# Kernel optimization log

Measured on AMD Instinct MI355X. Metric: run time of the kernel, lower is better.

Reference implementation:

```python
import jax, jax.numpy as jnp
import numpy as np

B = 1048576      # batch
D = 6            # action dim (x[0]..x[5] in the cvxpy program)
SDIM = 17        # state dim (s[11]..s[16] used)
CAP = 20.0       # constraint radius
BIG = 1e30


def setup_inputs() -> dict:
    key = jax.random.key(0)
    k1, k2 = jax.random.split(key)
    x = jax.random.normal(k1, (B, D), dtype=jnp.float32)
    s = jax.random.normal(k2, (B, SDIM), dtype=jnp.float32)
    return {"x": x, "s": s}


def _project_weighted_l1(q, s):
    # QP: argmin_x 0.5||x||^2 - q^T x  s.t.  sum_i |s[11+i]| * |x_i| <= CAP
    # == Euclidean projection of q onto weighted-L1 ball {x : sum_i w_i|x_i| <= CAP}
    # Closed form: x_i = sign(q_i) * max(|q_i| - lam * w_i, 0), lam >= 0 chosen so
    # constraint is tight (lam = 0 if q is already feasible).
    w = jnp.abs(s[:, 11:11 + D])                       # [B,D] weights
    a = jnp.abs(q)                                     # [B,D]
    sgn = jnp.sign(q)
    total = jnp.sum(w * a, axis=-1, keepdims=True)     # [B,1] constraint value at x=q

    # breakpoints r_i = |q_i| / w_i (coord i active iff r_i > lam); w_i==0 => always q_i
    w_safe = jnp.where(w > 0, w, 1.0)
    r = jnp.where(w > 0, a / w_safe, jnp.float32(BIG))  # [B,D]

    order = jnp.argsort(-r, axis=-1)                   # descending breakpoints
    r_s = jnp.take_along_axis(r, order, axis=-1)
    w_s = jnp.take_along_axis(w, order, axis=-1)
    a_s = jnp.take_along_axis(a, order, axis=-1)

    cum_wq = jnp.cumsum(w_s * a_s, axis=-1)            # [B,D]
    cum_w2 = jnp.cumsum(w_s * w_s, axis=-1)            # [B,D]
    cum_w2_safe = jnp.where(cum_w2 > 0, cum_w2, 1.0)
    lam_k = (cum_wq - CAP) / cum_w2_safe               # candidate lam for prefix k+1

    valid = (r_s > lam_k) & (cum_w2 > 0)               # prefix-monotone validity
    k_star = jnp.maximum(jnp.sum(valid.astype(jnp.int32), axis=-1, keepdims=True) - 1, 0)
    lam = jnp.take_along_axis(lam_k, k_star, axis=-1)  # [B,1]
    lam = jnp.where(total > CAP, jnp.maximum(lam, 0.0), 0.0)

    return sgn * jnp.maximum(a - lam * w, 0.0)         # [B,D]


def reference(x, s):
    return _project_weighted_l1(x, s)
```

## Files before the change

kernel.cpp:

```cpp
#include <hip/hip_runtime.h>

#define DD 6
#define SDIM 17
#define CAPF 20.0f
#define BIGF 1e30f
#define ROWS 256

__global__ __launch_bounds__(256) void proj_wl1_kernel(
    const float* __restrict__ x, const float* __restrict__ s,
    float* __restrict__ out, int B)
{
    __shared__ float ls[ROWS * SDIM];
    __shared__ float lx[ROWS * DD];

    const int tid = threadIdx.x;
    const size_t row0 = (size_t)blockIdx.x * ROWS;
    const bool full = (row0 + ROWS) <= (size_t)B;

    float q[DD], w[DD];

    if (full) {
        const float4* gs = reinterpret_cast<const float4*>(s + row0 * SDIM);
        float4* lsv = reinterpret_cast<float4*>(ls);
        for (int t = tid; t < ROWS * SDIM / 4; t += ROWS) lsv[t] = gs[t];

        const float4* gx = reinterpret_cast<const float4*>(x + row0 * DD);
        float4* lxv = reinterpret_cast<float4*>(lx);
        for (int t = tid; t < ROWS * DD / 4; t += ROWS) lxv[t] = gx[t];

        __syncthreads();

#pragma unroll
        for (int i = 0; i < DD; ++i) q[i] = lx[tid * DD + i];
#pragma unroll
        for (int i = 0; i < DD; ++i) w[i] = fabsf(ls[tid * SDIM + 11 + i]);
    } else {
        size_t row = row0 + tid;
        bool ok = row < (size_t)B;
        const float* xp = x + row * DD;
        const float* sp = s + row * SDIM + 11;
#pragma unroll
        for (int i = 0; i < DD; ++i) q[i] = ok ? xp[i] : 0.f;
#pragma unroll
        for (int i = 0; i < DD; ++i) w[i] = ok ? fabsf(sp[i]) : 0.f;
    }

    float a[DD], r[DD], wq[DD], w2[DD];
    float total = 0.f;
#pragma unroll
    for (int i = 0; i < DD; ++i) {
        a[i]  = fabsf(q[i]);
        wq[i] = w[i] * a[i];
        w2[i] = w[i] * w[i];
        total += wq[i];
        r[i]  = (w[i] > 0.f) ? (a[i] / w[i]) : BIGF;
    }

#pragma unroll
    for (int i = 0; i < DD - 1; ++i) {
#pragma unroll
        for (int j = 0; j < DD - 1 - i; ++j) {
            bool sw = r[j] < r[j + 1];
            float t0 = r[j], t1 = wq[j], t2 = w2[j];
            r[j]  = sw ? r[j + 1]  : r[j];
            wq[j] = sw ? wq[j + 1] : wq[j];
            w2[j] = sw ? w2[j + 1] : w2[j];
            r[j + 1]  = sw ? t0 : r[j + 1];
            wq[j + 1] = sw ? t1 : wq[j + 1];
            w2[j + 1] = sw ? t2 : w2[j + 1];
        }
    }

    float cwq = 0.f, cw2 = 0.f;
    float lamk[DD];
    int m = 0;
#pragma unroll
    for (int k = 0; k < DD; ++k) {
        cwq += wq[k];
        cw2 += w2[k];
        float safe = (cw2 > 0.f) ? cw2 : 1.f;
        lamk[k] = (cwq - CAPF) / safe;
        bool valid = (r[k] > lamk[k]) && (cw2 > 0.f);
        m += valid ? 1 : 0;
    }
    int ks = m - 1;
    if (ks < 0) ks = 0;
    float lam = lamk[0];
#pragma unroll
    for (int k = 1; k < DD; ++k) lam = (ks == k) ? lamk[k] : lam;
    lam = (total > CAPF) ? fmaxf(lam, 0.f) : 0.f;

    float o[DD];
#pragma unroll
    for (int i = 0; i < DD; ++i) {
        float mag = fmaxf(a[i] - lam * w[i], 0.f);
        float sgn = (q[i] > 0.f) ? 1.f : ((q[i] < 0.f) ? -1.f : 0.f);
        o[i] = sgn * mag;
    }

    if (full) {
        __syncthreads();
#pragma unroll
        for (int i = 0; i < DD; ++i) lx[tid * DD + i] = o[i];
        __syncthreads();

        float4* gout = reinterpret_cast<float4*>(out + row0 * DD);
        const float4* lxv = reinterpret_cast<const float4*>(lx);
        for (int t = tid; t < ROWS * DD / 4; t += ROWS) gout[t] = lxv[t];
    } else {
        size_t row = row0 + tid;
        if (row < (size_t)B) {
            float* op = out + row * DD;
#pragma unroll
            for (int i = 0; i < DD; ++i) op[i] = o[i];
        }
    }
}

extern "C" void kernel_launch(void* const* d_in, const int* in_sizes, int n_in,
                              void* d_out, int out_size, void* d_ws, size_t ws_size,
                              hipStream_t stream)
{
    const float* x = (const float*)d_in[0];
    const float* s = (const float*)d_in[1];
    float* out = (float*)d_out;
    int B = in_sizes[0] / DD;

    const int block = ROWS;
    int grid = (B + block - 1) / block;
    proj_wl1_kernel<<<grid, block, 0, stream>>>(x, s, out, B);
}
```

Baseline: 26.78 us.

## Use per-wavefront LDS slabs and drop block barriers; load x directly as float2

Each 64-lane wavefront now stages its own 64 rows of s in a private LDS slab and reuses that slab for the output transpose. This removes all block-wide __syncthreads in favour of s_waitcnt, relying on wavefront lockstep execution for ordering. x is read straight from global memory as three float2 loads per thread instead of being staged through LDS. The aim is to cut barrier stalls and LDS traffic, but it depends on wave64 execution and on manual waitcnt being enough for correctness, and the strided float2 reads of x coalesce less well.

Result: no change. 26.93 us (+0.6%).

```diff
diff --git a/kernel.cpp b/kernel.cpp
--- a/kernel.cpp
+++ b/kernel.cpp
@@ -5,37 +5,46 @@
 #define CAPF 20.0f
 #define BIGF 1e30f
 #define ROWS 256
+#define WSLAB 1088
 
 __global__ __launch_bounds__(256) void proj_wl1_kernel(
     const float* __restrict__ x, const float* __restrict__ s,
     float* __restrict__ out, int B)
 {
-    __shared__ float ls[ROWS * SDIM];
-    __shared__ float lx[ROWS * DD];
+    __shared__ float lds[4 * WSLAB];
 
-    const int tid = threadIdx.x;
-    const size_t row0 = (size_t)blockIdx.x * ROWS;
+    const int tid  = threadIdx.x;
+    const int wv   = tid >> 6;
+    const int lane = tid & 63;
+    const size_t row0  = (size_t)blockIdx.x * ROWS;
+    const size_t wrow0 = row0 + (size_t)wv * 64;
     const bool full = (row0 + ROWS) <= (size_t)B;
 
+    float* lsw = lds + wv * WSLAB;
     float q[DD], w[DD];
 
     if (full) {
-        const float4* gs = reinterpret_cast<const float4*>(s + row0 * SDIM);
-        float4* lsv = reinterpret_cast<float4*>(ls);
-        for (int t = tid; t < ROWS * SDIM / 4; t += ROWS) lsv[t] = gs[t];
+        const float4* gs  = reinterpret_cast<const float4*>(s + wrow0 * SDIM);
+        float4* lsw4      = reinterpret_cast<float4*>(lsw);
+#pragma unroll
+        for (int it = 0; it < 4; ++it)
+            lsw4[it * 64 + lane] = gs[it * 64 + lane];
+        if (lane < 16)
+            lsw4[256 + lane] = gs[256 + lane];
 
-        const float4* gx = reinterpret_cast<const float4*>(x + row0 * DD);
-        float4* lxv = reinterpret_cast<float4*>(lx);
-        for (int t = tid; t < ROWS * DD / 4; t += ROWS) lxv[t] = gx[t];
+        const float* xp = x + (wrow0 + lane) * DD;
+        float2 q01 = *reinterpret_cast<const float2*>(xp + 0);
+        float2 q23 = *reinterpret_cast<const float2*>(xp + 2);
+        float2 q45 = *reinterpret_cast<const float2*>(xp + 4);
+        q[0] = q01.x; q[1] = q01.y; q[2] = q23.x;
+        q[3] = q23.y; q[4] = q45.x; q[5] = q45.y;
 
-        __syncthreads();
-
+        asm volatile("s_waitcnt lgkmcnt(0)" ::: "memory");
 #pragma unroll
-        for (int i = 0; i < DD; ++i) q[i] = lx[tid * DD + i];
-#pragma unroll
-        for (int i = 0; i < DD; ++i) w[i] = fabsf(ls[tid * SDIM + 11 + i]);
+        for (int i = 0; i < DD; ++i)
+            w[i] = fabsf(lsw[lane * SDIM + 11 + i]);
     } else {
-        size_t row = row0 + tid;
+        size_t row = wrow0 + lane;
         bool ok = row < (size_t)B;
         const float* xp = x + row * DD;
         const float* sp = s + row * SDIM + 11;
@@ -99,16 +108,18 @@
     }
 
     if (full) {
-        __syncthreads();
 #pragma unroll
-        for (int i = 0; i < DD; ++i) lx[tid * DD + i] = o[i];
-        __syncthreads();
+        for (int i = 0; i < DD; ++i)
+            lsw[lane * DD + i] = o[i];
+        asm volatile("s_waitcnt lgkmcnt(0)" ::: "memory");
 
-        float4* gout = reinterpret_cast<float4*>(out + row0 * DD);
-        const float4* lxv = reinterpret_cast<const float4*>(lx);
-        for (int t = tid; t < ROWS * DD / 4; t += ROWS) gout[t] = lxv[t];
+        float4* go = reinterpret_cast<float4*>(out + wrow0 * DD);
+        const float4* lsw4 = reinterpret_cast<const float4*>(lsw);
+        go[lane] = lsw4[lane];
+        if (lane < 32)
+            go[64 + lane] = lsw4[64 + lane];
     } else {
-        size_t row = row0 + tid;
+        size_t row = wrow0 + lane;
         if (row < (size_t)B) {
             float* op = out + row * DD;
 #pragma unroll
```
